# Performance work log

Measured on AMD Instinct MI355X. Metric: run time of the kernel, lower is better.

## Reference

```python
import jax, jax.numpy as jnp
import numpy as np

H, O, E, V = 128, 128, 512, 34
B, T, L = 64, 2048, 256


def _lstm(x, wih, whh, bih, bhh):
    # x: [T, B, Din] -> outputs [T, B, H]; PyTorch gate order i, f, g, o
    n = whh.shape[1]
    h0 = jnp.zeros((x.shape[1], n), x.dtype)
    b = bih + bhh
    def step(carry, xt):
        h, c = carry
        g = xt @ wih.T + h @ whh.T + b
        i, f, gg, o = jnp.split(g, 4, axis=-1)
        c = jax.nn.sigmoid(f) * c + jax.nn.sigmoid(i) * jnp.tanh(gg)
        h = jax.nn.sigmoid(o) * jnp.tanh(c)
        return (h, c), h
    _, ys = jax.lax.scan(step, (h0, h0), x)
    return ys


def _conv1d_s2(x, w, b):
    # x: [B, Cin, T], w: [Cout, Cin, 2], kernel=2 stride=2 valid
    y = jax.lax.conv_general_dilated(x, w, (2,), 'VALID', dimension_numbers=('NCH', 'OIH', 'NCH'))
    return y + b[None, :, None]


def setup_inputs():
    key = jax.random.key(0)
    ctr = [0]
    def mk(shape, s=0.05):
        ctr[0] += 1
        return jax.random.normal(jax.random.fold_in(key, ctr[0]), shape, dtype=jnp.float32) * s
    inp = {}
    inp['utter'] = mk((B, T, 40), 1.0)
    inp['targets'] = jax.random.randint(jax.random.fold_in(key, 999), (B, L), 0, V)
    inp['wih_f'] = mk((4 * H, 40)); inp['whh_f'] = mk((4 * H, H)); inp['bih_f'] = mk((4 * H,)); inp['bhh_f'] = mk((4 * H,))
    inp['wih_r'] = mk((4 * H, 40)); inp['whh_r'] = mk((4 * H, H)); inp['bih_r'] = mk((4 * H,)); inp['bhh_r'] = mk((4 * H,))
    inp['c1w'] = mk((H, 2 * H, 2)); inp['c1b'] = mk((H,))
    inp['wih1'] = mk((4 * H, H)); inp['whh1'] = mk((4 * H, H)); inp['bih1'] = mk((4 * H,)); inp['bhh1'] = mk((4 * H,))
    inp['c2w'] = mk((H, H, 2)); inp['c2b'] = mk((H,))
    inp['wih2'] = mk((4 * H, H)); inp['whh2'] = mk((4 * H, H)); inp['bih2'] = mk((4 * H,)); inp['bhh2'] = mk((4 * H,))
    inp['kw'] = mk((O, H)); inp['kb'] = mk((O,)); inp['vw'] = mk((O, H)); inp['vb'] = mk((O,))
    inp['wihd'] = mk((4 * O, O + E)); inp['whhd'] = mk((4 * O, O)); inp['bihd'] = mk((4 * O,)); inp['bhhd'] = mk((4 * O,))
    inp['w1'] = mk((V, O)); inp['b1'] = mk((V,)); inp['w2'] = mk((V, O)); inp['b2'] = mk((V,))
    inp['w3'] = mk((V, V)); inp['b3'] = mk((V,))
    inp['emb'] = mk((V, E), 1.0)
    inp['sh0'] = mk((B, O)); inp['sc0'] = mk((B, O))
    return inp


def _forward(utter, targets, wih_f, whh_f, bih_f, bhh_f, wih_r, whh_r, bih_r, bhh_r,
             c1w, c1b, wih1, whh1, bih1, bhh1, c2w, c2b, wih2, whh2, bih2, bhh2,
             kw, kb, vw, vb, wihd, whhd, bihd, bhhd, w1, b1, w2, b2, w3, b3,
             emb, sh0, sc0):
    # ---- Listener (encoder) ----
    x = jnp.transpose(utter, (1, 0, 2))            # [T, B, 40]
    fwd = _lstm(x, wih_f, whh_f, bih_f, bhh_f)
    bwd = _lstm(x[::-1], wih_r, whh_r, bih_r, bhh_r)[::-1]
    h = jnp.concatenate([fwd, bwd], axis=-1)       # [T, B, 2H]
    h = jnp.transpose(h, (1, 2, 0))                # [B, 2H, T]
    h = _conv1d_s2(h, c1w, c1b)                    # [B, H, T/2]
    h = jnp.transpose(h, (2, 0, 1))                # [T/2, B, H]
    h = _lstm(h, wih1, whh1, bih1, bhh1)
    h = jnp.transpose(h, (1, 2, 0))
    h = _conv1d_s2(h, c2w, c2b)                    # [B, H, T/4]
    h = jnp.transpose(h, (2, 0, 1))
    h = _lstm(h, wih2, whh2, bih2, bhh2)
    h = jnp.transpose(h, (1, 0, 2))                # [B, T/4, H]
    hk = h @ kw.T + kb                              # [B, T/4, O]
    hv = h @ vw.T + vb
    # ---- Speller (decoder) ----
    ys = jnp.transpose(emb[targets], (1, 0, 2))[:-1]   # [L-1, B, E]
    mask = jnp.ones((utter.shape[0], hk.shape[1]), utter.dtype)  # all full-length
    bd = bihd + bhhd
    def step(carry, y_in):
        c, sh, sc = carry
        g = jnp.concatenate([y_in, c], axis=1) @ wihd.T + sh @ whhd.T + bd
        i, f, gg, o = jnp.split(g, 4, axis=-1)
        sc_n = jax.nn.sigmoid(f) * sc + jax.nn.sigmoid(i) * jnp.tanh(gg)
        sh_n = jax.nn.sigmoid(o) * jnp.tanh(sc_n)
        # NOTE: original attends with the cell state sc (faithful to source)
        att = jax.nn.softmax(jnp.einsum('btd,bd->bt', hk, sc_n), axis=1) * mask
        att = att / jnp.sum(att, axis=1, keepdims=True)
        c_n = jnp.einsum('bt,btd->bd', att, hv)
        out = jax.nn.relu(sh_n @ w1.T + b1 + c_n @ w2.T + b2)
        out = jax.nn.softmax(out @ w3.T + b3, axis=1)
        return (c_n, sh_n, sc_n), out
    c0 = jnp.zeros_like(sh0)
    _, preds = jax.lax.scan(step, (c0, sh0, sc0), ys)
    return jnp.transpose(preds, (1, 0, 2))         # [B, L-1, V]


def reference(utter, targets, wih_f, whh_f, bih_f, bhh_f, wih_r, whh_r, bih_r, bhh_r,
              c1w, c1b, wih1, whh1, bih1, bhh1, c2w, c2b, wih2, whh2, bih2, bhh2,
              kw, kb, vw, vb, wihd, whhd, bihd, bhhd, w1, b1, w2, b2, w3, b3,
              emb, sh0, sc0):
    return _forward(utter, targets, wih_f, whh_f, bih_f, bhh_f, wih_r, whh_r, bih_r, bhh_r,
                    c1w, c1b, wih1, whh1, bih1, bhh1, c2w, c2b, wih2, whh2, bih2, bhh2,
                    kw, kb, vw, vb, wihd, whhd, bihd, bhhd, w1, b1, w2, b2, w3, b3,
                    emb, sh0, sc0)
```

## Files before the change

### kernel.cpp

```cpp
#include <hip/hip_runtime.h>

typedef _Float16 half_t;
typedef _Float16 __attribute__((ext_vector_type(2))) half2_t;

__device__ __forceinline__ float fdot2_(half2_t a, half2_t b, float c) {
#if __has_builtin(__builtin_amdgcn_fdot2)
    return __builtin_amdgcn_fdot2(a, b, c, false);
#else
    return c + (float)a[0] * (float)b[0] + (float)a[1] * (float)b[1];
#endif
}
__device__ __forceinline__ half2_t h2(float a, float b) {
    half2_t r; r[0] = (half_t)a; r[1] = (half_t)b; return r;
}
__device__ __forceinline__ half2_t bc2(unsigned int u) {
    return __builtin_bit_cast(half2_t, u);
}
__device__ __forceinline__ unsigned int pk2(float a, float b) {
    return __builtin_bit_cast(unsigned int, h2(a, b));
}
__device__ __forceinline__ float sigm(float x) { return 1.0f / (1.0f + __expf(-x)); }
__device__ __forceinline__ float tanh_(float x) { return 1.0f - 2.0f / (1.0f + __expf(2.0f * x)); }
__device__ __forceinline__ unsigned int packbf2(float a, float b) {
    unsigned int ua = __float_as_uint(a);
    ua = (ua + 0x7fffu + ((ua >> 16) & 1u)) >> 16;
    unsigned int ub = __float_as_uint(b);
    ub = (ub + 0x7fffu + ((ub >> 16) & 1u)) >> 16;
    return ua | (ub << 16);
}
__device__ __forceinline__ float blo(unsigned int u) { return __uint_as_float(u << 16); }
__device__ __forceinline__ float bhi(unsigned int u) { return __uint_as_float(u & 0xffff0000u); }

__global__ __launch_bounds__(256) void packw_k(
    const float* __restrict__ src, unsigned int* __restrict__ dst, int cols, int nq)
{
    int g = blockIdx.x * 256 + threadIdx.x;
    if (g >= 512 * nq * 4) return;
    int k = g & 3, t = g >> 2;
    int tid = t & 511, q = t >> 9;
    int r = (tid & 3) * 128 + (tid >> 2);
    int col = (q * 4 + k) * 2;
    dst[g] = pk2(src[(size_t)r * cols + col], src[(size_t)r * cols + col + 1]);
}

__global__ __launch_bounds__(512, 1) void lstm1_k(
    const float* __restrict__ utter,
    const unsigned int* __restrict__ Whf, const unsigned int* __restrict__ Whr,
    const unsigned int* __restrict__ Wxf, const unsigned int* __restrict__ Wxr,
    const float* __restrict__ bih_f, const float* __restrict__ bhh_f,
    const float* __restrict__ bih_r, const float* __restrict__ bhh_r,
    unsigned short* __restrict__ Hf, unsigned short* __restrict__ Hr)
{
    const int tid = threadIdx.x;
    const int b = blockIdx.x & 63;
    const int dir = blockIdx.x >> 6;
    const unsigned int* Whp = dir ? Whr : Whf;
    const unsigned int* Wxp = dir ? Wxr : Wxf;
    const float* bih = dir ? bih_r : bih_f;
    const float* bhh = dir ? bhh_r : bhh_f;
    unsigned short* Hout = dir ? Hr : Hf;
    const int j = tid >> 2, gate = tid & 3;

    __shared__ __align__(16) half_t h_h[2][128];
    __shared__ __align__(16) half_t x2[2][8][48];
    __shared__ __align__(16) float ring[8][128];

    uint4 wh[16];
    {
        const uint4* W4 = reinterpret_cast<const uint4*>(Whp);
#pragma unroll
        for (int q = 0; q < 16; ++q) wh[q] = W4[q * 512 + tid];
    }
    uint4 wx[5];
    {
        const uint4* W4 = reinterpret_cast<const uint4*>(Wxp);
#pragma unroll
        for (int q = 0; q < 5; ++q) wx[q] = W4[q * 512 + tid];
    }
    const int r = gate * 128 + j;
    const float bias = bih[r] + bhh[r];
    float c = 0.0f;
    if (tid < 128) { h_h[0][tid] = (half_t)0.0f; }
    const int xs = tid / 40, xc = tid % 40;
    if (tid < 320) {
        int tt0 = dir ? (2047 - xs) : xs;
        x2[0][xs][xc] = (half_t)utter[((size_t)b * 2048 + tt0) * 40 + xc];
    }
    __syncthreads();

    for (int tc = 0; tc < 2048; tc += 8) {
        const int ph = (tc >> 3) & 1;
        float xreg = 0.0f;
        if (tid < 320) {
            int tn = tc + 8 + xs; if (tn > 2047) tn = 2047;
            int ttn = dir ? (2047 - tn) : tn;
            xreg = utter[((size_t)b * 2048 + ttn) * 40 + xc];
        }
#pragma unroll
        for (int s = 0; s < 8; ++s) {
            const int hb = (tc + s) & 1;
            float g0 = bias, g1 = 0.f, g2 = 0.f, g3 = 0.f;
            {
                const uint4* x4p = reinterpret_cast<const uint4*>(&x2[ph][s][0]);
#pragma unroll
                for (int q = 0; q < 5; ++q) {
                    uint4 u = x4p[q];
                    g0 = fdot2_(bc2(wx[q].x), bc2(u.x), g0);
                    g1 = fdot2_(bc2(wx[q].y), bc2(u.y), g1);
                    g2 = fdot2_(bc2(wx[q].z), bc2(u.z), g2);
                    g3 = fdot2_(bc2(wx[q].w), bc2(u.w), g3);
                }
                const uint4* h4p = reinterpret_cast<const uint4*>(&h_h[hb][0]);
#pragma unroll
                for (int q = 0; q < 16; ++q) {
                    uint4 u = h4p[q];
                    g0 = fdot2_(bc2(wh[q].x), bc2(u.x), g0);
                    g1 = fdot2_(bc2(wh[q].y), bc2(u.y), g1);
                    g2 = fdot2_(bc2(wh[q].z), bc2(u.z), g2);
                    g3 = fdot2_(bc2(wh[q].w), bc2(u.w), g3);
                }
            }
            float g = (g0 + g1) + (g2 + g3);
            float act = (gate == 2) ? tanh_(g) : sigm(g);
            float f_ = __shfl_xor(act, 1);
            float gg = __shfl_xor(act, 2);
            float o_ = __shfl_xor(act, 3);
            c = f_ * c + act * gg;
            float hh = o_ * tanh_(c);
            if (gate == 0) {
                h_h[hb ^ 1][j] = (half_t)hh;
                ring[s][j] = hh;
            }
            if (s == 7 && tid < 320)
                x2[ph ^ 1][xs][xc] = (half_t)xreg;
            __syncthreads();
        }
        {
            int s2 = tid >> 6, pr = tid & 63;
            int t = tc + s2;
            int tt = dir ? (2047 - t) : t;
            unsigned int v = pk2(ring[s2][2 * pr], ring[s2][2 * pr + 1]);
            reinterpret_cast<unsigned int*>(Hout)[((size_t)tt * 64 + b) * 64 + pr] = v;
        }
    }
}

__global__ __launch_bounds__(512, 1) void lstm_k(
    const unsigned short* __restrict__ Ph,
    const unsigned int* __restrict__ Wh,
    void* __restrict__ Hout, int T, int outHalf)
{
    const int tid = threadIdx.x;
    const int b = blockIdx.x;
    const int j = tid >> 2, gate = tid & 3;
    __shared__ __align__(16) half_t h_h[2][128];
    __shared__ __align__(16) float ring[8][128];
    uint4 wh[16];
    {
        const uint4* W4 = reinterpret_cast<const uint4*>(Wh);
#pragma unroll
        for (int q = 0; q < 16; ++q) wh[q] = W4[q * 512 + tid];
    }
    float c = 0.0f;
    if (tid < 128) h_h[0][tid] = (half_t)0.0f;
    const size_t pbase = (size_t)b * T;
    float pcur[8], pnext[8];
#pragma unroll
    for (int s = 0; s < 8; ++s)
        pcur[s] = (float)__builtin_bit_cast(half_t, Ph[(pbase + s) * 512 + tid]);
    __syncthreads();

    for (int tc = 0; tc < T; tc += 8) {
#pragma unroll
        for (int s = 0; s < 8; ++s) {
            int tn = tc + 8 + s; if (tn > T - 1) tn = T - 1;
            pnext[s] = (float)__builtin_bit_cast(half_t, Ph[(pbase + tn) * 512 + tid]);
        }
#pragma unroll
        for (int s = 0; s < 8; ++s) {
            const int hb = (tc + s) & 1;
            float g0 = pcur[s], g1 = 0.f, g2 = 0.f, g3 = 0.f;
            const uint4* h4p = reinterpret_cast<const uint4*>(&h_h[hb][0]);
#pragma unroll
            for (int q = 0; q < 16; ++q) {
                uint4 u = h4p[q];
                g0 = fdot2_(bc2(wh[q].x), bc2(u.x), g0);
                g1 = fdot2_(bc2(wh[q].y), bc2(u.y), g1);
                g2 = fdot2_(bc2(wh[q].z), bc2(u.z), g2);
                g3 = fdot2_(bc2(wh[q].w), bc2(u.w), g3);
            }
            float g = (g0 + g1) + (g2 + g3);
            float act = (gate == 2) ? tanh_(g) : sigm(g);
            float f_ = __shfl_xor(act, 1);
            float gg = __shfl_xor(act, 2);
            float o_ = __shfl_xor(act, 3);
            c = f_ * c + act * gg;
            float hh = o_ * tanh_(c);
            if (gate == 0) {
                h_h[hb ^ 1][j] = (half_t)hh;
                ring[s][j] = hh;
            }
            __syncthreads();
        }
        {
            int s2 = tid >> 6, pr = tid & 63;
            int t = tc + s2;
            if (outHalf) {
                unsigned int v = pk2(ring[s2][2 * pr], ring[s2][2 * pr + 1]);
                reinterpret_cast<unsigned int*>(Hout)[((size_t)t * 64 + b) * 64 + pr] = v;
            } else {
                float2 v = make_float2(ring[s2][2 * pr], ring[s2][2 * pr + 1]);
                *reinterpret_cast<float2*>(
                    &reinterpret_cast<float*>(Hout)[((size_t)t * 64 + b) * 128 + 2 * pr]) = v;
            }
        }
#pragma unroll
        for (int s = 0; s < 8; ++s) pcur[s] = pnext[s];
    }
}

template <int CIN>
__global__ __launch_bounds__(128) void conv_k(
    const unsigned short* __restrict__ HA, const unsigned short* __restrict__ HB,
    const float* __restrict__ W, const float* __restrict__ bias,
    float* __restrict__ out, int Tout)
{
    __shared__ __align__(16) float xin[64 * CIN];
    const int b = blockIdx.x;
    const int t0 = blockIdx.y * 32;
    const int tid = threadIdx.x;
    for (int idx = tid; idx < 64 * CIN; idx += 128) {
        int tl = idx / CIN, ci = idx % CIN;
        int tau = t0 * 2 + tl;
        unsigned short u;
        if constexpr (CIN == 256) {
            u = (ci < 128) ? HA[(size_t)tau * 8192 + b * 128 + ci]
                           : HB[(size_t)tau * 8192 + b * 128 + (ci - 128)];
        } else {
            u = HA[(size_t)tau * 8192 + b * 128 + ci];
        }
        xin[idx] = (float)__builtin_bit_cast(half_t, u);
    }
    __syncthreads();
    const int co = tid;
    float acc[32];
#pragma unroll
    for (int u = 0; u < 32; ++u) acc[u] = 0.0f;
    const float4* Wrow4 = reinterpret_cast<const float4*>(W + (size_t)co * 2 * CIN);
    const float4* xin4 = reinterpret_cast<const float4*>(xin);
    for (int c4 = 0; c4 < CIN / 4; ++c4) {
        float4 wA = Wrow4[2 * c4];
        float4 wB = Wrow4[2 * c4 + 1];
#pragma unroll
        for (int u = 0; u < 32; ++u) {
            float4 x0 = xin4[(2 * u) * (CIN / 4) + c4];
            float4 x1 = xin4[(2 * u + 1) * (CIN / 4) + c4];
            acc[u] += wA.x * x0.x + wA.y * x1.x + wA.z * x0.y + wA.w * x1.y
                    + wB.x * x0.z + wB.y * x1.z + wB.z * x0.w + wB.w * x1.w;
        }
    }
    float bs = bias[co];
#pragma unroll
    for (int u = 0; u < 32; ++u)
        out[((size_t)b * Tout + t0 + u) * 128 + co] = acc[u] + bs;
}

__global__ __launch_bounds__(256) void gemm_k(
    const float* __restrict__ A, const float* __restrict__ W, int ldw,
    const float* __restrict__ bias1, const float* __restrict__ bias2,
    void* __restrict__ C, int M, int N, int K, int mode, int Tdim)
{
    __shared__ __align__(16) float As[16][68];
    __shared__ __align__(16) float Ws[16][68];
    const int tid = threadIdx.x;
    const int m0 = blockIdx.x * 64, n0 = blockIdx.y * 64;
    const int kk = tid & 15, mm = tid >> 4;
    const int tm = tid & 15, tn = tid >> 4;
    float acc[4][4];
#pragma unroll
    for (int i = 0; i < 4; ++i)
#pragma unroll
        for (int jj = 0; jj < 4; ++jj) acc[i][jj] = 0.0f;

    for (int k0 = 0; k0 < K; k0 += 16) {
#pragma unroll
        for (int r = 0; r < 4; ++r) {
            As[kk][mm + 16 * r] = A[(size_t)(m0 + mm + 16 * r) * K + k0 + kk];
            Ws[kk][mm + 16 * r] = W[(size_t)(n0 + mm + 16 * r) * ldw + k0 + kk];
        }
        __syncthreads();
#pragma unroll
        for (int q = 0; q < 16; ++q) {
            float4 a = reinterpret_cast<const float4*>(&As[q][0])[tm];
            float4 w = reinterpret_cast<const float4*>(&Ws[q][0])[tn];
            acc[0][0] += a.x * w.x; acc[0][1] += a.x * w.y; acc[0][2] += a.x * w.z; acc[0][3] += a.x * w.w;
            acc[1][0] += a.y * w.x; acc[1][1] += a.y * w.y; acc[1][2] += a.y * w.z; acc[1][3] += a.y * w.w;
            acc[2][0] += a.z * w.x; acc[2][1] += a.z * w.y; acc[2][2] += a.z * w.z; acc[2][3] += a.z * w.w;
            acc[3][0] += a.w * w.x; acc[3][1] += a.w * w.y; acc[3][2] += a.w * w.z; acc[3][3] += a.w * w.w;
        }
        __syncthreads();
    }
    float bv[4];
#pragma unroll
    for (int jj = 0; jj < 4; ++jj) {
        int n = n0 + tn * 4 + jj;
        float v = 0.0f;
        if (bias1) v += bias1[n];
        if (bias2) v += bias2[n];
        bv[jj] = v;
    }
#pragma unroll
    for (int i = 0; i < 4; ++i) {
        int m = m0 + tm * 4 + i;
#pragma unroll
        for (int jj = 0; jj < 4; ++jj) {
            int n = n0 + tn * 4 + jj;
            float v = acc[i][jj] + bv[jj];
            if (mode == 0) {
                ((float*)C)[(size_t)m * N + n] = v;
            } else if (mode == 1) {
                int bb = m & 63, tt = m >> 6;
                ((float*)C)[((size_t)bb * N + n) * Tdim + tt] = v;
            } else if (mode == 2) {
                ((unsigned short*)C)[(size_t)m * N + n] =
                    __builtin_bit_cast(unsigned short, (half_t)v);
            } else {
                ((unsigned short*)C)[(size_t)m * 512 + (n & 127) * 4 + (n >> 7)] =
                    __builtin_bit_cast(unsigned short, (half_t)v);
            }
        }
    }
}

__global__ __launch_bounds__(512) void packemb_k(
    const int* __restrict__ targets, const float* __restrict__ emb,
    float* __restrict__ Ypack)
{
    int m = blockIdx.x;
    int l = m >> 6, b = m & 63;
    int tgt = targets[b * 256 + l];
    Ypack[(size_t)m * 512 + threadIdx.x] = emb[(size_t)tgt * 512 + threadIdx.x];
}

__global__ __launch_bounds__(256) void packq_k(
    const float* __restrict__ src, unsigned int* __restrict__ dst,
    int srcCols, int colOff, int nq, int rows)
{
    int g = blockIdx.x * 256 + threadIdx.x;
    if (g >= rows * nq * 4) return;
    int k = g & 3, t = g >> 2;
    int j = t % rows, q = t / rows;
    int p = q * 4 + k;
    const float* s = src + (size_t)j * srcCols + colOff + 2 * p;
    dst[g] = pk2(s[0], s[1]);
}

__global__ __launch_bounds__(1024) void packhv2_k(
    const float* __restrict__ hvT, unsigned int* __restrict__ hvq)
{
    int b = blockIdx.x;
    for (int it = 0; it < 32; ++it) {
        int idx = it * 1024 + threadIdx.x;
        int tq = idx >> 7, d = idx & 127;
        const float* s = hvT + ((size_t)b * 128 + d) * 512 + 2 * tq;
        hvq[(size_t)b * 32768 + idx] = packbf2(s[0], s[1]);
    }
}

__global__ __launch_bounds__(512, 1) void decoder_k(
    const float* __restrict__ Yp,
    const unsigned int* __restrict__ Wd,
    const float* __restrict__ hk,
    const unsigned int* __restrict__ hvq,
    const float* __restrict__ sh0, const float* __restrict__ sc0,
    float* __restrict__ SHs, float* __restrict__ Cs)
{
    __shared__ unsigned int hk_lds[512][66];
    __shared__ float acts[512];
    __shared__ float pfl[512];
    __shared__ __align__(16) half_t sh_h[128];
    __shared__ __align__(16) float sc_f[128];
    __shared__ __align__(16) half_t c_h[128];
    __shared__ __align__(16) float att[512];
    __shared__ float red[8];

    const int tid = threadIdx.x;
    const int b = blockIdx.x;
    const int gt = tid >> 7;

    uint4 wh[16];
    {
        const uint4* W4 = reinterpret_cast<const uint4*>(Wd);
#pragma unroll
        for (int q = 0; q < 16; ++q) wh[q] = W4[q * 512 + tid];
    }
    const uint4* Wc4 = reinterpret_cast<const uint4*>(Wd) + 8192;

    {
        const float4* hp = reinterpret_cast<const float4*>(hk + ((size_t)tid * 64 + b) * 128);
#pragma unroll
        for (int q = 0; q < 32; ++q) {
            float4 v = hp[q];
            hk_lds[tid][2 * q]     = packbf2(v.x, v.y);
            hk_lds[tid][2 * q + 1] = packbf2(v.z, v.w);
        }
    }
    float sc_r = 0.0f;
    if (tid < 128) {
        sh_h[tid] = (half_t)sh0[b * 128 + tid];
        sc_r = sc0[b * 128 + tid];
        sc_f[tid] = sc_r;
        c_h[tid] = (half_t)0.0f;
    }
    __syncthreads();

    const int wid = tid >> 6, lane = tid & 63;
    const int g4 = tid >> 7, d = tid & 127;
    const unsigned int* hvp = hvq + (size_t)b * 32768 + (size_t)(g4 * 64) * 128 + d;
    const float2* att2 = reinterpret_cast<const float2*>(att);
    float yp_cur = Yp[(size_t)b * 512 + tid];

    for (int l = 0; l < 255; ++l) {
        int lnxt = (l + 1 < 255) ? (l + 1) : l;
        float yp_nxt = Yp[((size_t)lnxt * 64 + b) * 512 + tid];
        {
            float g0 = yp_cur, g1 = 0.f, g2 = 0.f, g3 = 0.f;
            const uint4* s4 = reinterpret_cast<const uint4*>(sh_h);
#pragma unroll
            for (int q = 0; q < 16; ++q) {
                uint4 u = s4[q];
                g0 = fdot2_(bc2(wh[q].x), bc2(u.x), g0);
                g1 = fdot2_(bc2(wh[q].y), bc2(u.y), g1);
                g2 = fdot2_(bc2(wh[q].z), bc2(u.z), g2);
                g3 = fdot2_(bc2(wh[q].w), bc2(u.w), g3);
            }
            const uint4* c4 = reinterpret_cast<const uint4*>(c_h);
#pragma unroll
            for (int q = 0; q < 16; ++q) {
                uint4 w = Wc4[q * 512 + tid];
                uint4 u = c4[q];
                g0 = fdot2_(bc2(w.x), bc2(u.x), g0);
                g1 = fdot2_(bc2(w.y), bc2(u.y), g1);
                g2 = fdot2_(bc2(w.z), bc2(u.z), g2);
                g3 = fdot2_(bc2(w.w), bc2(u.w), g3);
            }
            float g = (g0 + g1) + (g2 + g3);
            acts[tid] = (gt == 2) ? tanh_(g) : sigm(g);
        }
        __syncthreads();
        if (tid < 128) {
            float i_ = acts[tid];
            float f_ = acts[128 + tid];
            float g_ = acts[256 + tid];
            float o_ = acts[384 + tid];
            sc_r = f_ * sc_r + i_ * g_;
            float hh = o_ * tanh_(sc_r);
            sh_h[tid] = (half_t)hh;
            sc_f[tid] = sc_r;
            SHs[((size_t)l * 64 + b) * 128 + tid] = hh;
        }
        __syncthreads();
        {
            float e0 = 0.f, e1 = 0.f, e2 = 0.f, e3 = 0.f;
            const uint2* hkr = reinterpret_cast<const uint2*>(&hk_lds[tid][0]);
            const float4* sc4 = reinterpret_cast<const float4*>(sc_f);
#pragma unroll
            for (int q = 0; q < 32; ++q) {
                uint2 u = hkr[q];
                float4 s = sc4[q];
                e0 += blo(u.x) * s.x; e1 += bhi(u.x) * s.y;
                e2 += blo(u.y) * s.z; e3 += bhi(u.y) * s.w;
            }
            float p = __expf((e0 + e1) + (e2 + e3));
            att[tid] = p;
            float ps = p;
#pragma unroll
            for (int off = 32; off; off >>= 1) ps += __shfl_xor(ps, off);
            if (lane == 0) red[wid] = ps;
        }
        __syncthreads();
        {
            float a0 = 0.f, a1 = 0.f;
#pragma unroll 8
            for (int i = 0; i < 64; i += 2) {
                unsigned int u0 = hvp[(size_t)i * 128];
                unsigned int u1 = hvp[(size_t)(i + 1) * 128];
                float2 w0 = att2[g4 * 64 + i];
                float2 w1 = att2[g4 * 64 + i + 1];
                a0 += blo(u0) * w0.x + bhi(u0) * w0.y;
                a1 += blo(u1) * w1.x + bhi(u1) * w1.y;
            }
            pfl[tid] = a0 + a1;
        }
        __syncthreads();
        if (tid < 128) {
            float S = ((red[0] + red[1]) + (red[2] + red[3]))
                    + ((red[4] + red[5]) + (red[6] + red[7]));
            float cv = (pfl[tid] + pfl[128 + tid] + pfl[256 + tid] + pfl[384 + tid]) / S;
            c_h[tid] = (half_t)cv;
            Cs[((size_t)l * 64 + b) * 128 + tid] = cv;
        }
        yp_cur = yp_nxt;
        __syncthreads();
    }
}

__global__ __launch_bounds__(256) void mlp_k(
    const float* __restrict__ SHs, const float* __restrict__ Cs,
    const float* __restrict__ w1, const float* __restrict__ b1,
    const float* __restrict__ w2, const float* __restrict__ b2,
    const float* __restrict__ w3, const float* __restrict__ b3,
    float* __restrict__ out)
{
    __shared__ float o_l[4][34];
    const int sub = threadIdx.x >> 6, lane = threadIdx.x & 63;
    const int m = blockIdx.x * 4 + sub;
    const int l = m >> 6, b = m & 63;
    if (lane < 34) {
        float o1 = b1[lane] + b2[lane];
        const float4* w1r = reinterpret_cast<const float4*>(w1 + lane * 128);
        const float4* w2r = reinterpret_cast<const float4*>(w2 + lane * 128);
        const float4* sh4 = reinterpret_cast<const float4*>(SHs + (size_t)m * 128);
        const float4* c4  = reinterpret_cast<const float4*>(Cs + (size_t)m * 128);
#pragma unroll 8
        for (int q = 0; q < 32; ++q) {
            float4 a = w1r[q], h = sh4[q], w = w2r[q], cc = c4[q];
            o1 += a.x * h.x + a.y * h.y + a.z * h.z + a.w * h.w
                + w.x * cc.x + w.y * cc.y + w.z * cc.z + w.w * cc.w;
        }
        o_l[sub][lane] = fmaxf(o1, 0.0f);
    }
    __syncthreads();
    if (lane < 34) {
        float zz = b3[lane];
        const float* w3r = w3 + lane * 34;
        for (int v = 0; v < 34; ++v) zz += w3r[v] * o_l[sub][v];
        __syncthreads();
        o_l[sub][lane] = zz;
        __syncthreads();
        float zm = o_l[sub][0];
        for (int v = 1; v < 34; ++v) zm = fmaxf(zm, o_l[sub][v]);
        float Ssum = 0.0f;
        for (int v = 0; v < 34; ++v) Ssum += __expf(o_l[sub][v] - zm);
        out[((size_t)b * 255 + l) * 34 + lane] = __expf(zz - zm) / Ssum;
    }
}

extern "C" void kernel_launch(void* const* d_in, const int* in_sizes, int n_in,
                              void* d_out, int out_size, void* d_ws, size_t ws_size,
                              hipStream_t stream) {
    (void)in_sizes; (void)n_in; (void)out_size; (void)ws_size;
    const float* utter = (const float*)d_in[0];
    const int*   targets = (const int*)d_in[1];
    const float* wih_f = (const float*)d_in[2];
    const float* whh_f = (const float*)d_in[3];
    const float* bih_f = (const float*)d_in[4];
    const float* bhh_f = (const float*)d_in[5];
    const float* wih_r = (const float*)d_in[6];
    const float* whh_r = (const float*)d_in[7];
    const float* bih_r = (const float*)d_in[8];
    const float* bhh_r = (const float*)d_in[9];
    const float* c1w = (const float*)d_in[10];
    const float* c1b = (const float*)d_in[11];
    const float* wih1 = (const float*)d_in[12];
    const float* whh1 = (const float*)d_in[13];
    const float* bih1 = (const float*)d_in[14];
    const float* bhh1 = (const float*)d_in[15];
    const float* c2w = (const float*)d_in[16];
    const float* c2b = (const float*)d_in[17];
    const float* wih2 = (const float*)d_in[18];
    const float* whh2 = (const float*)d_in[19];
    const float* bih2 = (const float*)d_in[20];
    const float* bhh2 = (const float*)d_in[21];
    const float* kw = (const float*)d_in[22];
    const float* kb = (const float*)d_in[23];
    const float* vw = (const float*)d_in[24];
    const float* vb = (const float*)d_in[25];
    const float* wihd = (const float*)d_in[26];
    const float* whhd = (const float*)d_in[27];
    const float* bihd = (const float*)d_in[28];
    const float* bhhd = (const float*)d_in[29];
    const float* w1 = (const float*)d_in[30];
    const float* b1 = (const float*)d_in[31];
    const float* w2 = (const float*)d_in[32];
    const float* b2 = (const float*)d_in[33];
    const float* w3 = (const float*)d_in[34];
    const float* b3 = (const float*)d_in[35];
    const float* emb = (const float*)d_in[36];
    const float* sh0 = (const float*)d_in[37];
    const float* sc0 = (const float*)d_in[38];

    char* ws = (char*)d_ws;
    const size_t MB = 1ull << 20;
    unsigned int* W = (unsigned int*)(ws + 0);
    unsigned int* Wd   = W + 0;
    unsigned int* Wl1f = W + 65536;
    unsigned int* Wl1r = W + 98304;
    unsigned int* Wl2  = W + 131072;
    unsigned int* Wl3  = W + 163840;
    unsigned int* Wxf  = W + 196608;
    unsigned int* Wxr  = W + 206848;

    unsigned short* Hf_h   = (unsigned short*)(ws + 1 * MB);
    unsigned short* Hr_h   = (unsigned short*)(ws + 33 * MB);
    float*          conv1o = (float*)(ws + 65 * MB);
    unsigned short* P2_h   = (unsigned short*)(ws + 1 * MB);
    unsigned short* H2_h   = (unsigned short*)(ws + 65 * MB);
    float*          conv2o = (float*)(ws + 81 * MB);
    unsigned short* P3_h   = (unsigned short*)(ws + 97 * MB);
    float*          H3     = (float*)(ws + 1 * MB);
    float*          hkb    = (float*)(ws + 17 * MB);
    float*          hvT    = (float*)(ws + 33 * MB);
    unsigned int*   hvq    = (unsigned int*)(ws + 49 * MB);
    float*          Ypack  = (float*)(ws + 57 * MB);
    float*          Yp     = (float*)(ws + 89 * MB);
    float*          SHsave = (float*)(ws + 121 * MB);
    float*          Csave  = (float*)(ws + 130 * MB);

    packq_k<<<128, 256, 0, stream>>>(whhd, Wd + 0,     128, 0,   16, 512);
    packq_k<<<128, 256, 0, stream>>>(wihd, Wd + 32768, 640, 512, 16, 512);
    packw_k<<<128, 256, 0, stream>>>(whh_f, Wl1f, 128, 16);
    packw_k<<<128, 256, 0, stream>>>(whh_r, Wl1r, 128, 16);
    packw_k<<<128, 256, 0, stream>>>(whh1, Wl2, 128, 16);
    packw_k<<<128, 256, 0, stream>>>(whh2, Wl3, 128, 16);
    packw_k<<<40, 256, 0, stream>>>(wih_f, Wxf, 40, 5);
    packw_k<<<40, 256, 0, stream>>>(wih_r, Wxr, 40, 5);

    lstm1_k<<<128, 512, 0, stream>>>(utter, Wl1f, Wl1r, Wxf, Wxr,
                                     bih_f, bhh_f, bih_r, bhh_r, Hf_h, Hr_h);
    conv_k<256><<<dim3(64, 32), 128, 0, stream>>>(Hf_h, Hr_h, c1w, c1b, conv1o, 1024);
    gemm_k<<<dim3(1024, 8), 256, 0, stream>>>(conv1o, wih1, 128, bih1, bhh1,
                                              P2_h, 65536, 512, 128, 3, 0);
    lstm_k<<<64, 512, 0, stream>>>(P2_h, Wl2, H2_h, 1024, 1);
    conv_k<128><<<dim3(64, 16), 128, 0, stream>>>(H2_h, nullptr, c2w, c2b, conv2o, 512);
    gemm_k<<<dim3(512, 8), 256, 0, stream>>>(conv2o, wih2, 128, bih2, bhh2,
                                             P3_h, 32768, 512, 128, 3, 0);
    lstm_k<<<64, 512, 0, stream>>>(P3_h, Wl3, H3, 512, 0);
    gemm_k<<<dim3(512, 2), 256, 0, stream>>>(H3, kw, 128, kb, nullptr,
                                             hkb, 32768, 128, 128, 0, 0);
    gemm_k<<<dim3(512, 2), 256, 0, stream>>>(H3, vw, 128, vb, nullptr,
                                             hvT, 32768, 128, 128, 1, 512);
    packhv2_k<<<64, 1024, 0, stream>>>(hvT, hvq);
    packemb_k<<<16320, 512, 0, stream>>>(targets, emb, Ypack);
    gemm_k<<<dim3(255, 8), 256, 0, stream>>>(Ypack, wihd, 640, bihd, bhhd,
                                             Yp, 16320, 512, 512, 0, 0);
    decoder_k<<<64, 512, 0, stream>>>(Yp, Wd, hkb, hvq, sh0, sc0, SHsave, Csave);
    mlp_k<<<4080, 256, 0, stream>>>(SHsave, Csave, w1, b1, w2, b2, w3, b3, (float*)d_out);
}
```

Before: 5.241 ms.

## Overlap decoder embedding GEMM with first LSTM using spare blocks; batch decoder stores

The embedding-gather plus wihd projection GEMM for the decoder input is moved into extra blocks of the first LSTM kernel launch (blocks 128-191). There it runs concurrently with the latency-bound recurrence on otherwise idle CUs, which removes the separate packemb and GEMM launches and the Ypack buffer. The decoder now prefetches 8 Yp rows per chunk and buffers the SH/C outputs in LDS rings, writing them in batches. Workspace offsets are reshuffled so Yp survives until the decoder runs. The risks are that the union-shared LDS may lower occupancy and that the fused GEMM uses a simple fp32 tile loop.

```diff
diff --git a/kernel.cpp b/kernel.cpp
--- a/kernel.cpp
+++ b/kernel.cpp
@@ -49,9 +49,74 @@
     const unsigned int* __restrict__ Wxf, const unsigned int* __restrict__ Wxr,
     const float* __restrict__ bih_f, const float* __restrict__ bhh_f,
     const float* __restrict__ bih_r, const float* __restrict__ bhh_r,
-    unsigned short* __restrict__ Hf, unsigned short* __restrict__ Hr)
-{
+    unsigned short* __restrict__ Hf, unsigned short* __restrict__ Hr,
+    const int* __restrict__ targets, const float* __restrict__ emb,
+    const float* __restrict__ wihd, const float* __restrict__ bihd,
+    const float* __restrict__ bhhd, float* __restrict__ Yp)
+{
+    __shared__ __align__(16) union {
+        struct { half_t h_h[2][128]; half_t x2[2][8][48]; float ring[8][128]; } l;
+        struct { float As[2][16][68]; float Ws[2][16][68]; } g;
+    } sm;
     const int tid = threadIdx.x;
+
+    if (blockIdx.x >= 128) {
+        const int half = tid >> 8, ht = tid & 255;
+        float (*As)[68] = sm.g.As[half];
+        float (*Ws)[68] = sm.g.Ws[half];
+        const int kk = ht & 15, mm = ht >> 4;
+        const int tm = ht & 15, tn = ht >> 4;
+        const int base = (blockIdx.x - 128) * 2 + half;
+        for (int it = 0; it < 16; ++it) {
+            int tile = base + it * 128;
+            bool active = tile < 2040;
+            int t2 = active ? tile : 0;
+            int n0 = (t2 & 7) * 64, m0 = (t2 >> 3) * 64;
+            const float* arow[4];
+#pragma unroll
+            for (int r = 0; r < 4; ++r) {
+                int m = m0 + mm + 16 * r;
+                int l = m >> 6, bb = m & 63;
+                arow[r] = emb + (size_t)targets[bb * 256 + l] * 512;
+            }
+            float acc[4][4];
+#pragma unroll
+            for (int i = 0; i < 4; ++i)
+#pragma unroll
+                for (int jj = 0; jj < 4; ++jj) acc[i][jj] = 0.0f;
+            for (int k0 = 0; k0 < 512; k0 += 16) {
+#pragma unroll
+                for (int r = 0; r < 4; ++r) {
+                    As[kk][mm + 16 * r] = arow[r][k0 + kk];
+                    Ws[kk][mm + 16 * r] = wihd[(size_t)(n0 + mm + 16 * r) * 640 + k0 + kk];
+                }
+                __syncthreads();
+#pragma unroll
+                for (int q = 0; q < 16; ++q) {
+                    float4 a = reinterpret_cast<const float4*>(&As[q][0])[tm];
+                    float4 w = reinterpret_cast<const float4*>(&Ws[q][0])[tn];
+                    acc[0][0] += a.x * w.x; acc[0][1] += a.x * w.y; acc[0][2] += a.x * w.z; acc[0][3] += a.x * w.w;
+                    acc[1][0] += a.y * w.x; acc[1][1] += a.y * w.y; acc[1][2] += a.y * w.z; acc[1][3] += a.y * w.w;
+                    acc[2][0] += a.z * w.x; acc[2][1] += a.z * w.y; acc[2][2] += a.z * w.z; acc[2][3] += a.z * w.w;
+                    acc[3][0] += a.w * w.x; acc[3][1] += a.w * w.y; acc[3][2] += a.w * w.z; acc[3][3] += a.w * w.w;
+                }
+                __syncthreads();
+            }
+            if (active) {
+#pragma unroll
+                for (int i = 0; i < 4; ++i) {
+                    int m = m0 + tm * 4 + i;
+#pragma unroll
+                    for (int jj = 0; jj < 4; ++jj) {
+                        int n = n0 + tn * 4 + jj;
+                        Yp[(size_t)m * 512 + n] = acc[i][jj] + bihd[n] + bhhd[n];
+                    }
+                }
+            }
+        }
+        return;
+    }
+
     const int b = blockIdx.x & 63;
     const int dir = blockIdx.x >> 6;
     const unsigned int* Whp = dir ? Whr : Whf;
@@ -61,10 +126,6 @@
     unsigned short* Hout = dir ? Hr : Hf;
     const int j = tid >> 2, gate = tid & 3;
 
-    __shared__ __align__(16) half_t h_h[2][128];
-    __shared__ __align__(16) half_t x2[2][8][48];
-    __shared__ __align__(16) float ring[8][128];
-
     uint4 wh[16];
     {
         const uint4* W4 = reinterpret_cast<const uint4*>(Whp);
@@ -80,11 +141,11 @@
     const int r = gate * 128 + j;
     const float bias = bih[r] + bhh[r];
     float c = 0.0f;
-    if (tid < 128) { h_h[0][tid] = (half_t)0.0f; }
+    if (tid < 128) { sm.l.h_h[0][tid] = (half_t)0.0f; }
     const int xs = tid / 40, xc = tid % 40;
     if (tid < 320) {
         int tt0 = dir ? (2047 - xs) : xs;
-        x2[0][xs][xc] = (half_t)utter[((size_t)b * 2048 + tt0) * 40 + xc];
+        sm.l.x2[0][xs][xc] = (half_t)utter[((size_t)b * 2048 + tt0) * 40 + xc];
     }
     __syncthreads();
 
@@ -101,7 +162,7 @@
             const int hb = (tc + s) & 1;
             float g0 = bias, g1 = 0.f, g2 = 0.f, g3 = 0.f;
             {
-                const uint4* x4p = reinterpret_cast<const uint4*>(&x2[ph][s][0]);
+                const uint4* x4p = reinterpret_cast<const uint4*>(&sm.l.x2[ph][s][0]);
 #pragma unroll
                 for (int q = 0; q < 5; ++q) {
                     uint4 u = x4p[q];
@@ -110,7 +171,7 @@
                     g2 = fdot2_(bc2(wx[q].z), bc2(u.z), g2);
                     g3 = fdot2_(bc2(wx[q].w), bc2(u.w), g3);
                 }
-                const uint4* h4p = reinterpret_cast<const uint4*>(&h_h[hb][0]);
+                const uint4* h4p = reinterpret_cast<const uint4*>(&sm.l.h_h[hb][0]);
 #pragma unroll
                 for (int q = 0; q < 16; ++q) {
                     uint4 u = h4p[q];
@@ -128,18 +189,18 @@
             c = f_ * c + act * gg;
             float hh = o_ * tanh_(c);
             if (gate == 0) {
-                h_h[hb ^ 1][j] = (half_t)hh;
-                ring[s][j] = hh;
+                sm.l.h_h[hb ^ 1][j] = (half_t)hh;
+                sm.l.ring[s][j] = hh;
             }
             if (s == 7 && tid < 320)
-                x2[ph ^ 1][xs][xc] = (half_t)xreg;
+                sm.l.x2[ph ^ 1][xs][xc] = (half_t)xreg;
             __syncthreads();
         }
         {
             int s2 = tid >> 6, pr = tid & 63;
             int t = tc + s2;
             int tt = dir ? (2047 - t) : t;
-            unsigned int v = pk2(ring[s2][2 * pr], ring[s2][2 * pr + 1]);
+            unsigned int v = pk2(sm.l.ring[s2][2 * pr], sm.l.ring[s2][2 * pr + 1]);
             reinterpret_cast<unsigned int*>(Hout)[((size_t)tt * 64 + b) * 64 + pr] = v;
         }
     }
@@ -332,16 +393,6 @@
     }
 }
 
-__global__ __launch_bounds__(512) void packemb_k(
-    const int* __restrict__ targets, const float* __restrict__ emb,
-    float* __restrict__ Ypack)
-{
-    int m = blockIdx.x;
-    int l = m >> 6, b = m & 63;
-    int tgt = targets[b * 256 + l];
-    Ypack[(size_t)m * 512 + threadIdx.x] = emb[(size_t)tgt * 512 + threadIdx.x];
-}
-
 __global__ __launch_bounds__(256) void packq_k(
     const float* __restrict__ src, unsigned int* __restrict__ dst,
     int srcCols, int colOff, int nq, int rows)
@@ -383,6 +434,8 @@
     __shared__ __align__(16) half_t c_h[128];
     __shared__ __align__(16) float att[512];
     __shared__ float red[8];
+    __shared__ __align__(16) float ringSH[8][128];
+    __shared__ __align__(16) float ringC[8][128];
 
     const int tid = threadIdx.x;
     const int b = blockIdx.x;
@@ -418,90 +471,100 @@
     const int g4 = tid >> 7, d = tid & 127;
     const unsigned int* hvp = hvq + (size_t)b * 32768 + (size_t)(g4 * 64) * 128 + d;
     const float2* att2 = reinterpret_cast<const float2*>(att);
-    float yp_cur = Yp[(size_t)b * 512 + tid];
-
-    for (int l = 0; l < 255; ++l) {
-        int lnxt = (l + 1 < 255) ? (l + 1) : l;
-        float yp_nxt = Yp[((size_t)lnxt * 64 + b) * 512 + tid];
-        {
-            float g0 = yp_cur, g1 = 0.f, g2 = 0.f, g3 = 0.f;
-            const uint4* s4 = reinterpret_cast<const uint4*>(sh_h);
-#pragma unroll
-            for (int q = 0; q < 16; ++q) {
-                uint4 u = s4[q];
-                g0 = fdot2_(bc2(wh[q].x), bc2(u.x), g0);
-                g1 = fdot2_(bc2(wh[q].y), bc2(u.y), g1);
-                g2 = fdot2_(bc2(wh[q].z), bc2(u.z), g2);
-                g3 = fdot2_(bc2(wh[q].w), bc2(u.w), g3);
-            }
-            const uint4* c4 = reinterpret_cast<const uint4*>(c_h);
-#pragma unroll
-            for (int q = 0; q < 16; ++q) {
-                uint4 w = Wc4[q * 512 + tid];
-                uint4 u = c4[q];
-                g0 = fdot2_(bc2(w.x), bc2(u.x), g0);
-                g1 = fdot2_(bc2(w.y), bc2(u.y), g1);
-                g2 = fdot2_(bc2(w.z), bc2(u.z), g2);
-                g3 = fdot2_(bc2(w.w), bc2(u.w), g3);
-            }
-            float g = (g0 + g1) + (g2 + g3);
-            acts[tid] = (gt == 2) ? tanh_(g) : sigm(g);
-        }
-        __syncthreads();
-        if (tid < 128) {
-            float i_ = acts[tid];
-            float f_ = acts[128 + tid];
-            float g_ = acts[256 + tid];
-            float o_ = acts[384 + tid];
-            sc_r = f_ * sc_r + i_ * g_;
-            float hh = o_ * tanh_(sc_r);
-            sh_h[tid] = (half_t)hh;
-            sc_f[tid] = sc_r;
-            SHs[((size_t)l * 64 + b) * 128 + tid] = hh;
-        }
-        __syncthreads();
-        {
-            float e0 = 0.f, e1 = 0.f, e2 = 0.f, e3 = 0.f;
-            const uint2* hkr = reinterpret_cast<const uint2*>(&hk_lds[tid][0]);
-            const float4* sc4 = reinterpret_cast<const float4*>(sc_f);
-#pragma unroll
-            for (int q = 0; q < 32; ++q) {
-                uint2 u = hkr[q];
-                float4 s = sc4[q];
-                e0 += blo(u.x) * s.x; e1 += bhi(u.x) * s.y;
-                e2 += blo(u.y) * s.z; e3 += bhi(u.y) * s.w;
-            }
-            float p = __expf((e0 + e1) + (e2 + e3));
-            att[tid] = p;
-            float ps = p;
-#pragma unroll
-            for (int off = 32; off; off >>= 1) ps += __shfl_xor(ps, off);
-            if (lane == 0) red[wid] = ps;
-        }
-        __syncthreads();
-        {
-            float a0 = 0.f, a1 = 0.f;
+
+    for (int lc = 0; lc < 255; lc += 8) {
+        const int ns = (255 - lc < 8) ? (255 - lc) : 8;
+        float ypv[8];
+#pragma unroll
+        for (int s = 0; s < 8; ++s) {
+            int ll = lc + s; if (ll > 254) ll = 254;
+            ypv[s] = Yp[((size_t)ll * 64 + b) * 512 + tid];
+        }
+        for (int s = 0; s < ns; ++s) {
+            {
+                float g0 = 0.f, g1 = 0.f, g2 = 0.f, g3 = 0.f;
+                const uint4* s4 = reinterpret_cast<const uint4*>(sh_h);
+#pragma unroll
+                for (int q = 0; q < 16; ++q) {
+                    uint4 u = s4[q];
+                    g0 = fdot2_(bc2(wh[q].x), bc2(u.x), g0);
+                    g1 = fdot2_(bc2(wh[q].y), bc2(u.y), g1);
+                    g2 = fdot2_(bc2(wh[q].z), bc2(u.z), g2);
+                    g3 = fdot2_(bc2(wh[q].w), bc2(u.w), g3);
+                }
+                const uint4* c4 = reinterpret_cast<const uint4*>(c_h);
+#pragma unroll
+                for (int q = 0; q < 16; ++q) {
+                    uint4 w = Wc4[q * 512 + tid];
+                    uint4 u = c4[q];
+                    g0 = fdot2_(bc2(w.x), bc2(u.x), g0);
+                    g1 = fdot2_(bc2(w.y), bc2(u.y), g1);
+                    g2 = fdot2_(bc2(w.z), bc2(u.z), g2);
+                    g3 = fdot2_(bc2(w.w), bc2(u.w), g3);
+                }
+                float g = (g0 + g1) + (g2 + g3) + ypv[s];
+                acts[tid] = (gt == 2) ? tanh_(g) : sigm(g);
+            }
+            __syncthreads();
+            if (tid < 128) {
+                float i_ = acts[tid];
+                float f_ = acts[128 + tid];
+                float g_ = acts[256 + tid];
+                float o_ = acts[384 + tid];
+                sc_r = f_ * sc_r + i_ * g_;
+                float hh = o_ * tanh_(sc_r);
+                sh_h[tid] = (half_t)hh;
+                sc_f[tid] = sc_r;
+                ringSH[s][tid] = hh;
+            }
+            __syncthreads();
+            {
+                float e0 = 0.f, e1 = 0.f, e2 = 0.f, e3 = 0.f;
+                const uint2* hkr = reinterpret_cast<const uint2*>(&hk_lds[tid][0]);
+                const float4* sc4 = reinterpret_cast<const float4*>(sc_f);
+#pragma unroll
+                for (int q = 0; q < 32; ++q) {
+                    uint2 u = hkr[q];
+                    float4 sv = sc4[q];
+                    e0 += blo(u.x) * sv.x; e1 += bhi(u.x) * sv.y;
+                    e2 += blo(u.y) * sv.z; e3 += bhi(u.y) * sv.w;
+                }
+                float p = __expf((e0 + e1) + (e2 + e3));
+                att[tid] = p;
+                float ps = p;
+#pragma unroll
+                for (int off = 32; off; off >>= 1) ps += __shfl_xor(ps, off);
+                if (lane == 0) red[wid] = ps;
+            }
+            __syncthreads();
+            {
+                float a0 = 0.f, a1 = 0.f;
 #pragma unroll 8
-            for (int i = 0; i < 64; i += 2) {
-                unsigned int u0 = hvp[(size_t)i * 128];
-                unsigned int u1 = hvp[(size_t)(i + 1) * 128];
-                float2 w0 = att2[g4 * 64 + i];
-                float2 w1 = att2[g4 * 64 + i + 1];
-                a0 += blo(u0) * w0.x + bhi(u0) * w0.y;
-                a1 += blo(u1) * w1.x + bhi(u1) * w1.y;
-            }
-            pfl[tid] = a0 + a1;
-        }
-        __syncthreads();
-        if (tid < 128) {
-            float S = ((red[0] + red[1]) + (red[2] + red[3]))
-                    + ((red[4] + red[5]) + (red[6] + red[7]));
-            float cv = (pfl[tid] + pfl[128 + tid] + pfl[256 + tid] + pfl[384 + tid]) / S;
-            c_h[tid] = (half_t)cv;
-            Cs[((size_t)l * 64 + b) * 128 + tid] = cv;
-        }
-        yp_cur = yp_nxt;
-        __syncthreads();
+                for (int i = 0; i < 64; i += 2) {
+                    unsigned int u0 = hvp[(size_t)i * 128];
+                    unsigned int u1 = hvp[(size_t)(i + 1) * 128];
+                    float2 w0 = att2[g4 * 64 + i];
+                    float2 w1 = att2[g4 * 64 + i + 1];
+                    a0 += blo(u0) * w0.x + bhi(u0) * w0.y;
+                    a1 += blo(u1) * w1.x + bhi(u1) * w1.y;
+                }
+                pfl[tid] = a0 + a1;
+            }
+            __syncthreads();
+            if (tid < 128) {
+                float S = ((red[0] + red[1]) + (red[2] + red[3]))
+                        + ((red[4] + red[5]) + (red[6] + red[7]));
+                float cv = (pfl[tid] + pfl[128 + tid] + pfl[256 + tid] + pfl[384 + tid]) / S;
+                c_h[tid] = (half_t)cv;
+                ringC[s][tid] = cv;
+            }
+            __syncthreads();
+        }
+        for (int idx = tid; idx < ns * 128; idx += 512) {
+            int s2 = idx >> 7, dd = idx & 127;
+            SHs[((size_t)(lc + s2) * 64 + b) * 128 + dd] = ringSH[s2][dd];
+            Cs[((size_t)(lc + s2) * 64 + b) * 128 + dd] = ringC[s2][dd];
+        }
     }
 }
 
@@ -603,17 +666,16 @@
 
     unsigned short* Hf_h   = (unsigned short*)(ws + 1 * MB);
     unsigned short* Hr_h   = (unsigned short*)(ws + 33 * MB);
-    float*          conv1o = (float*)(ws + 65 * MB);
+    float*          Yp     = (float*)(ws + 65 * MB);
+    float*          conv1o = (float*)(ws + 97 * MB);
     unsigned short* P2_h   = (unsigned short*)(ws + 1 * MB);
-    unsigned short* H2_h   = (unsigned short*)(ws + 65 * MB);
-    float*          conv2o = (float*)(ws + 81 * MB);
-    unsigned short* P3_h   = (unsigned short*)(ws + 97 * MB);
-    float*          H3     = (float*)(ws + 1 * MB);
-    float*          hkb    = (float*)(ws + 17 * MB);
-    float*          hvT    = (float*)(ws + 33 * MB);
-    unsigned int*   hvq    = (unsigned int*)(ws + 49 * MB);
-    float*          Ypack  = (float*)(ws + 57 * MB);
-    float*          Yp     = (float*)(ws + 89 * MB);
+    unsigned short* H2_h   = (unsigned short*)(ws + 97 * MB);
+    float*          conv2o = (float*)(ws + 113 * MB);
+    unsigned short* P3_h   = (unsigned short*)(ws + 1 * MB);
+    float*          H3     = (float*)(ws + 33 * MB);
+    float*          hkb    = (float*)(ws + 49 * MB);
+    float*          hvT    = (float*)(ws + 97 * MB);
+    unsigned int*   hvq    = (unsigned int*)(ws + 113 * MB);
     float*          SHsave = (float*)(ws + 121 * MB);
     float*          Csave  = (float*)(ws + 130 * MB);
 
@@ -626,8 +688,9 @@
     packw_k<<<40, 256, 0, stream>>>(wih_f, Wxf, 40, 5);
     packw_k<<<40, 256, 0, stream>>>(wih_r, Wxr, 40, 5);
 
-    lstm1_k<<<128, 512, 0, stream>>>(utter, Wl1f, Wl1r, Wxf, Wxr,
-                                     bih_f, bhh_f, bih_r, bhh_r, Hf_h, Hr_h);
+    lstm1_k<<<192, 512, 0, stream>>>(utter, Wl1f, Wl1r, Wxf, Wxr,
+                                     bih_f, bhh_f, bih_r, bhh_r, Hf_h, Hr_h,
+                                     targets, emb, wihd, bihd, bhhd, Yp);
     conv_k<256><<<dim3(64, 32), 128, 0, stream>>>(Hf_h, Hr_h, c1w, c1b, conv1o, 1024);
     gemm_k<<<dim3(1024, 8), 256, 0, stream>>>(conv1o, wih1, 128, bih1, bhh1,
                                               P2_h, 65536, 512, 128, 3, 0);
@@ -641,9 +704,6 @@
     gemm_k<<<dim3(512, 2), 256, 0, stream>>>(H3, vw, 128, vb, nullptr,
                                              hvT, 32768, 128, 128, 1, 512);
     packhv2_k<<<64, 1024, 0, stream>>>(hvT, hvq);
-    packemb_k<<<16320, 512, 0, stream>>>(targets, emb, Ypack);
-    gemm_k<<<dim3(255, 8), 256, 0, stream>>>(Ypack, wihd, 640, bihd, bhhd,
-                                             Yp, 16320, 512, 512, 0, 0);
     decoder_k<<<64, 512, 0, stream>>>(Yp, Wd, hkb, hvq, sh0, sc0, SHsave, Csave);
     mlp_k<<<4080, 256, 0, stream>>>(SHsave, Csave, w1, b1, w2, b2, w3, b3, (float*)d_out);
 }
```

New measurement: 5.181 ms. Within noise of the previous version (-1.1%).
